# Kernel optimization log

Hardware: AMD Instinct MI355X
Metric: run time of the kernel (lower is better)

## Reference

```python
import jax, jax.numpy as jnp
import numpy as np

EPS = 1e-9
ROUTING_ITERS = 3


def _squash_elem(s):
    # Faithful to source: squash over trailing axis of size 1 => elementwise.
    sq = s * s
    return (sq / (1.0 + sq)) * s / jnp.sqrt(sq + EPS)


def setup_inputs() -> dict:
    key = jax.random.key(0)
    k1, k2 = jax.random.split(key)
    B, I, P = 16, 2048, 16   # batch, num_input_capsules, input_dim_capsules
    O, D = 64, 32            # num_capsules, dim_capsules
    x = jax.random.normal(k1, (B, I, P), dtype=jnp.float32)
    # glorot-ish scale for the transformation weights
    W = jax.random.normal(k2, (1, I, O, D, P), dtype=jnp.float32) * (1.0 / np.sqrt(P))
    bias = jnp.zeros((1, 1, O, D, 1), dtype=jnp.float32)
    return {"x": x, "W": W, "bias": bias}


def reference(x, W, bias):
    # u_hat[b,i,o,d] = sum_p W[0,i,o,d,p] * x[b,i,p]  (the tile+mul+reduce in TF)
    u_hat = jnp.einsum('bip,iodp->biod', x, W[0])
    B, I, O, _ = u_hat.shape
    bias_od = bias[0, 0, :, :, 0]               # [O, D]
    b_logits = jnp.zeros((B, I, O), dtype=u_hat.dtype)
    v = None
    for it in range(ROUTING_ITERS):
        c = jax.nn.softmax(b_logits, axis=2)     # softmax over output capsules
        s = jnp.einsum('bio,biod->bod', c, u_hat) + bias_od
        v = _squash_elem(s)                      # [B, O, D]
        if it < ROUTING_ITERS - 1:
            # agreement[b,i,o] = sum_d u_hat[b,i,o,d] * v[b,o,d]
            b_logits = b_logits + jnp.einsum('biod,bod->bio', u_hat, v)
    return v  # [B, num_capsules, dim_capsules]
```

## Files before the change

kernel.cpp:

```cpp
#include <hip/hip_runtime.h>
#include <hip/hip_bf16.h>

#define B_ 16
#define I_ 2048
#define P_ 16
#define O_ 64
#define D_ 32
#define OD_ 2048
#define EPSQ 1e-9f

__device__ __forceinline__ float squashf(float s) {
  float sq = s * s;
  return sq / (1.0f + sq) * s * rsqrtf(sq + EPSQ);
}

__global__ __launch_bounds__(256) void k_uhat(
    const float* __restrict__ x, const float* __restrict__ W,
    float* __restrict__ u)
{
  const int t = threadIdx.x;
  const int q = blockIdx.x & 3;
  const int i0 = (blockIdx.x >> 2) * 8;
  const int pr = q * 256 + t;

  for (int ii = 0; ii < 8; ++ii) {
    const int i = i0 + ii;
    const float4* wp = (const float4*)(W + (size_t)(i * OD_ + pr * 2) * P_);
    float4 w[8];
#pragma unroll
    for (int k = 0; k < 8; ++k) w[k] = wp[k];

#pragma unroll
    for (int b = 0; b < B_; ++b) {
      const float4* xp = (const float4*)(x + (size_t)(b * I_ + i) * P_);
      float u0 = 0.f, u1 = 0.f;
#pragma unroll
      for (int qq = 0; qq < 4; ++qq) {
        float4 xq = xp[qq];
        float4 wa = w[qq], wb = w[qq + 4];
        u0 += xq.x * wa.x + xq.y * wa.y + xq.z * wa.z + xq.w * wa.w;
        u1 += xq.x * wb.x + xq.y * wb.y + xq.z * wb.z + xq.w * wb.w;
      }
      float2 uv; uv.x = u0; uv.y = u1;
      *(float2*)(u + (size_t)(b * I_ + i) * OD_ + pr * 2) = uv;
    }
  }
}

__global__ __launch_bounds__(256) void k_s0sum(
    const float* __restrict__ u, float* __restrict__ s0)
{
  const int t = threadIdx.x;
  const int ic = blockIdx.x & 15;
  const int b = (blockIdx.x >> 4) & 15;
  const int od = (blockIdx.x >> 8) * 256 + t;
  float a = 0.f;
  const float* p = u + (size_t)(b * I_ + ic * 128) * OD_ + od;
  for (int k = 0; k < 128; ++k) a += p[(size_t)k * OD_];
  atomicAdd(&s0[b * OD_ + od], a);
}

__global__ __launch_bounds__(256, 3) void k_route(
    const float* __restrict__ u,
    const float* __restrict__ sA, float scaleA,
    const float* __restrict__ sB,
    const float* __restrict__ bias,
    float* __restrict__ s_out)
{
  __shared__ float red[4 * 2048];
  const int t = threadIdx.x;
  const int o = t & 63;
  const int wv = t >> 6;
  const int b = blockIdx.x >> 6;
  const int i0 = ((blockIdx.x & 63) * 4 + wv) * 8;

  float vv[32];
  {
    const int base = b * OD_ + o * 32;
#pragma unroll
    for (int d = 0; d < 32; ++d) {
      float bs = bias[o * 32 + d];
      float val = squashf(sA[base + d] * scaleA + bs);
      if (sB) val += squashf(sB[base + d] + bs);
      vv[d] = val;
    }
  }
  float acc[32];
#pragma unroll
  for (int d = 0; d < 32; ++d) acc[d] = 0.f;

  for (int ii = 0; ii < 8; ++ii) {
    const int i = i0 + ii;
    const float4* up = (const float4*)(u + (size_t)(b * I_ + i) * OD_ + o * 32);
    float uf[32];
#pragma unroll
    for (int qq = 0; qq < 8; ++qq) {
      float4 r = up[qq];
      uf[4 * qq + 0] = r.x; uf[4 * qq + 1] = r.y;
      uf[4 * qq + 2] = r.z; uf[4 * qq + 3] = r.w;
    }
    float logit = 0.f;
#pragma unroll
    for (int d = 0; d < 32; ++d) logit = fmaf(uf[d], vv[d], logit);
    float m = logit;
#pragma unroll
    for (int off = 32; off > 0; off >>= 1) m = fmaxf(m, __shfl_xor(m, off, 64));
    float e = __expf(logit - m);
    float sm = e;
#pragma unroll
    for (int off = 32; off > 0; off >>= 1) sm += __shfl_xor(sm, off, 64);
    float c = e / sm;
#pragma unroll
    for (int d = 0; d < 32; ++d) acc[d] = fmaf(c, uf[d], acc[d]);
  }

#pragma unroll
  for (int d = 0; d < 32; ++d) red[wv * 2048 + d * 64 + o] = acc[d];
  __syncthreads();
#pragma unroll
  for (int k = 0; k < 8; ++k) {
    int od = t * 8 + k;
    int oo = od >> 5, dd = od & 31;
    int a = dd * 64 + oo;
    float r = red[a] + red[2048 + a] + red[4096 + a] + red[6144 + a];
    atomicAdd(&s_out[b * OD_ + od], r);
  }
}

__global__ void k_out(const float* __restrict__ s2, const float* __restrict__ bias,
                      float* __restrict__ out)
{
  int j = blockIdx.x * 256 + threadIdx.x;
  out[j] = squashf(s2[j] + bias[j & (OD_ - 1)]);
}

extern "C" void kernel_launch(void* const* d_in, const int* in_sizes, int n_in,
                              void* d_out, int out_size, void* d_ws, size_t ws_size,
                              hipStream_t stream) {
  const float* x = (const float*)d_in[0];
  const float* W = (const float*)d_in[1];
  const float* bias = (const float*)d_in[2];
  float* out = (float*)d_out;

  char* ws = (char*)d_ws;
  float* u_ws = (float*)ws;
  float* s0 = (float*)(ws + 268435456ull);
  float* s1 = s0 + 32768;
  float* s2 = s1 + 32768;

  hipMemsetAsync(s0, 0, 3 * 32768 * sizeof(float), stream);
  k_uhat<<<dim3(1024), dim3(256), 0, stream>>>(x, W, u_ws);
  k_s0sum<<<dim3(2048), dim3(256), 0, stream>>>(u_ws, s0);
  k_route<<<dim3(1024), dim3(256), 0, stream>>>(u_ws, s0, 1.0f / 64.0f, nullptr, bias, s1);
  k_route<<<dim3(1024), dim3(256), 0, stream>>>(u_ws, s0, 1.0f / 64.0f, s1, bias, s2);
  k_out<<<dim3(128), dim3(256), 0, stream>>>(s2, bias, out);
}
```

Measured before the change: 675.0 us.

## Fuse s0 column sums into u_hat kernel and replace atomics with partial-sum reductions

The first-iteration sum over input capsules is now accumulated in registers inside the u_hat kernel and written as per-chunk partials. This removes a separate pass that re-read the whole 256 MB u_hat buffer. The routing kernels write per-block partials instead of doing atomicAdd into s, and small reduction kernels combine them deterministically, which also removes the memset. The cost is extra register pressure in k_uhat, two more small launches, and about 50 MB of partial buffers.

```diff
diff --git a/kernel.cpp b/kernel.cpp
--- a/kernel.cpp
+++ b/kernel.cpp
@@ -1,11 +1,7 @@
 #include <hip/hip_runtime.h>
-#include <hip/hip_bf16.h>
 
 #define B_ 16
 #define I_ 2048
-#define P_ 16
-#define O_ 64
-#define D_ 32
 #define OD_ 2048
 #define EPSQ 1e-9f
 
@@ -16,23 +12,28 @@
 
 __global__ __launch_bounds__(256) void k_uhat(
     const float* __restrict__ x, const float* __restrict__ W,
-    float* __restrict__ u)
+    float* __restrict__ u, float* __restrict__ part0)
 {
   const int t = threadIdx.x;
   const int q = blockIdx.x & 3;
-  const int i0 = (blockIdx.x >> 2) * 8;
+  const int ic = blockIdx.x >> 2;
+  const int i0 = ic * 8;
   const int pr = q * 256 + t;
+
+  float s0a[B_], s0b[B_];
+#pragma unroll
+  for (int b = 0; b < B_; ++b) { s0a[b] = 0.f; s0b[b] = 0.f; }
 
   for (int ii = 0; ii < 8; ++ii) {
     const int i = i0 + ii;
-    const float4* wp = (const float4*)(W + (size_t)(i * OD_ + pr * 2) * P_);
+    const float4* wp = (const float4*)(W + (size_t)(i * OD_ + pr * 2) * 16);
     float4 w[8];
 #pragma unroll
     for (int k = 0; k < 8; ++k) w[k] = wp[k];
 
 #pragma unroll
     for (int b = 0; b < B_; ++b) {
-      const float4* xp = (const float4*)(x + (size_t)(b * I_ + i) * P_);
+      const float4* xp = (const float4*)(x + (size_t)(b * I_ + i) * 16);
       float u0 = 0.f, u1 = 0.f;
 #pragma unroll
       for (int qq = 0; qq < 4; ++qq) {
@@ -43,21 +44,25 @@
       }
       float2 uv; uv.x = u0; uv.y = u1;
       *(float2*)(u + (size_t)(b * I_ + i) * OD_ + pr * 2) = uv;
+      s0a[b] += u0; s0b[b] += u1;
     }
+  }
+#pragma unroll
+  for (int b = 0; b < B_; ++b) {
+    float2 sv; sv.x = s0a[b]; sv.y = s0b[b];
+    ((float2*)part0)[(size_t)(ic * B_ + b) * 1024 + pr] = sv;
   }
 }
 
-__global__ __launch_bounds__(256) void k_s0sum(
-    const float* __restrict__ u, float* __restrict__ s0)
+__global__ __launch_bounds__(256) void k_s0red(
+    const float* __restrict__ part0, float* __restrict__ s0)
 {
-  const int t = threadIdx.x;
-  const int ic = blockIdx.x & 15;
-  const int b = (blockIdx.x >> 4) & 15;
-  const int od = (blockIdx.x >> 8) * 256 + t;
+  const int b = blockIdx.x >> 3;
+  const int od = (blockIdx.x & 7) * 256 + threadIdx.x;
   float a = 0.f;
-  const float* p = u + (size_t)(b * I_ + ic * 128) * OD_ + od;
-  for (int k = 0; k < 128; ++k) a += p[(size_t)k * OD_];
-  atomicAdd(&s0[b * OD_ + od], a);
+  const float* p = part0 + (size_t)b * OD_ + od;
+  for (int ic = 0; ic < 256; ++ic) a += p[(size_t)ic * B_ * OD_];
+  s0[b * OD_ + od] = a;
 }
 
 __global__ __launch_bounds__(256, 3) void k_route(
@@ -65,7 +70,7 @@
     const float* __restrict__ sA, float scaleA,
     const float* __restrict__ sB,
     const float* __restrict__ bias,
-    float* __restrict__ s_out)
+    float* __restrict__ part)
 {
   __shared__ float red[4 * 2048];
   const int t = threadIdx.x;
@@ -122,16 +127,34 @@
     int od = t * 8 + k;
     int oo = od >> 5, dd = od & 31;
     int a = dd * 64 + oo;
-    float r = red[a] + red[2048 + a] + red[4096 + a] + red[6144 + a];
-    atomicAdd(&s_out[b * OD_ + od], r);
+    part[(size_t)blockIdx.x * OD_ + od] =
+        red[a] + red[2048 + a] + red[4096 + a] + red[6144 + a];
   }
 }
 
-__global__ void k_out(const float* __restrict__ s2, const float* __restrict__ bias,
-                      float* __restrict__ out)
+__global__ __launch_bounds__(256) void k_s1red(
+    const float* __restrict__ part, float* __restrict__ s1)
 {
-  int j = blockIdx.x * 256 + threadIdx.x;
-  out[j] = squashf(s2[j] + bias[j & (OD_ - 1)]);
+  const int b = blockIdx.x >> 3;
+  const int od = (blockIdx.x & 7) * 256 + threadIdx.x;
+  float a = 0.f;
+  const float* p = part + (size_t)b * 64 * OD_ + od;
+#pragma unroll 4
+  for (int g = 0; g < 64; ++g) a += p[(size_t)g * OD_];
+  s1[b * OD_ + od] = a;
+}
+
+__global__ __launch_bounds__(256) void k_outred(
+    const float* __restrict__ part, const float* __restrict__ bias,
+    float* __restrict__ out)
+{
+  const int b = blockIdx.x >> 3;
+  const int od = (blockIdx.x & 7) * 256 + threadIdx.x;
+  float a = 0.f;
+  const float* p = part + (size_t)b * 64 * OD_ + od;
+#pragma unroll 4
+  for (int g = 0; g < 64; ++g) a += p[(size_t)g * OD_];
+  out[b * OD_ + od] = squashf(a + bias[od]);
 }
 
 extern "C" void kernel_launch(void* const* d_in, const int* in_sizes, int n_in,
@@ -143,15 +166,17 @@
   float* out = (float*)d_out;
 
   char* ws = (char*)d_ws;
-  float* u_ws = (float*)ws;
-  float* s0 = (float*)(ws + 268435456ull);
-  float* s1 = s0 + 32768;
-  float* s2 = s1 + 32768;
+  float* u_ws  = (float*)ws;
+  float* part0 = (float*)(ws + 268435456ull);
+  float* part1 = (float*)(ws + 302055424ull);
+  float* part2 = (float*)(ws + 310444032ull);
+  float* s0    = (float*)(ws + 318832640ull);
+  float* s1    = s0 + 32768;
 
-  hipMemsetAsync(s0, 0, 3 * 32768 * sizeof(float), stream);
-  k_uhat<<<dim3(1024), dim3(256), 0, stream>>>(x, W, u_ws);
-  k_s0sum<<<dim3(2048), dim3(256), 0, stream>>>(u_ws, s0);
-  k_route<<<dim3(1024), dim3(256), 0, stream>>>(u_ws, s0, 1.0f / 64.0f, nullptr, bias, s1);
-  k_route<<<dim3(1024), dim3(256), 0, stream>>>(u_ws, s0, 1.0f / 64.0f, s1, bias, s2);
-  k_out<<<dim3(128), dim3(256), 0, stream>>>(s2, bias, out);
+  k_uhat <<<dim3(1024), dim3(256), 0, stream>>>(x, W, u_ws, part0);
+  k_s0red<<<dim3(128),  dim3(256), 0, stream>>>(part0, s0);
+  k_route<<<dim3(1024), dim3(256), 0, stream>>>(u_ws, s0, 1.0f / 64.0f, nullptr, bias, part1);
+  k_s1red<<<dim3(128),  dim3(256), 0, stream>>>(part1, s1);
+  k_route<<<dim3(1024), dim3(256), 0, stream>>>(u_ws, s0, 1.0f / 64.0f, s1, bias, part2);
+  k_outred<<<dim3(128), dim3(256), 0, stream>>>(part2, bias, out);
 }
```

After: 622.7 us. 1.08x faster.
